# Performance work log

Measured on AMD Instinct MI355X. Metric: run time of the kernel, lower is better.

Reference implementation:

```python
import jax, jax.numpy as jnp
import numpy as np

B, T = 512, 64
STOCH, DETER, HIDDEN = 30, 200, 200
A, EMBED = 12, 1024
MIN_STD = 0.1
UPDATE_BIAS = -1.0


def _linear_init(key, fan_in, fan_out):
    w_key, b_key = jax.random.split(key)
    lim = 1.0 / np.sqrt(fan_in)
    W = jax.random.uniform(w_key, (fan_in, fan_out), minval=-lim, maxval=lim, dtype=jnp.float32)
    b = jax.random.uniform(b_key, (fan_out,), minval=-lim, maxval=lim, dtype=jnp.float32)
    return W, b


def setup_inputs() -> dict:
    key = jax.random.key(0)
    ks = jax.random.split(key, 12)
    embed = jax.random.normal(ks[0], (B, T, EMBED), dtype=jnp.float32)
    action = jax.random.normal(ks[1], (B, T, A), dtype=jnp.float32)
    noise_prior = jax.random.normal(ks[2], (B, T, STOCH), dtype=jnp.float32)
    noise_post = jax.random.normal(ks[3], (B, T, STOCH), dtype=jnp.float32)
    inp_W, inp_b = _linear_init(ks[4], STOCH + A, HIDDEN)          # _inp_layers
    gru_W, gru_b = _linear_init(ks[5], HIDDEN + DETER, 3 * DETER)  # GRUCell._layer
    img_out_W, img_out_b = _linear_init(ks[6], DETER, HIDDEN)      # _img_out_layers
    ims_W, ims_b = _linear_init(ks[7], HIDDEN, 2 * STOCH)          # _ims_stat_layer
    obs_out_W, obs_out_b = _linear_init(ks[8], DETER + EMBED, HIDDEN)  # _obs_out_layers
    obs_W, obs_b = _linear_init(ks[9], HIDDEN, 2 * STOCH)          # _obs_stat_layer
    return dict(embed=embed, action=action, noise_prior=noise_prior, noise_post=noise_post,
                inp_W=inp_W, inp_b=inp_b, gru_W=gru_W, gru_b=gru_b,
                img_out_W=img_out_W, img_out_b=img_out_b, ims_W=ims_W, ims_b=ims_b,
                obs_out_W=obs_out_W, obs_out_b=obs_out_b, obs_W=obs_W, obs_b=obs_b)


def _observe(embed, action, noise_prior, noise_post,
             inp_W, inp_b, gru_W, gru_b, img_out_W, img_out_b,
             ims_W, ims_b, obs_out_W, obs_out_b, obs_W, obs_b):
    # time-major for scan: [T, B, ...]
    emb_t = jnp.swapaxes(embed, 0, 1)
    act_t = jnp.swapaxes(action, 0, 1)
    npr_t = jnp.swapaxes(noise_prior, 0, 1)
    npo_t = jnp.swapaxes(noise_post, 0, 1)

    def step(carry, xs):
        stoch, deter = carry                    # posterior stoch [B,STOCH], deter [B,DETER]
        a, e, nz_pr, nz_po = xs
        # img_step: input MLP
        x = jax.nn.elu(jnp.concatenate([stoch, a], -1) @ inp_W + inp_b)
        # GRUCell (norm=False)
        parts = jnp.concatenate([x, deter], -1) @ gru_W + gru_b   # [B, 3*DETER]
        reset, cand, update = jnp.split(parts, 3, -1)
        reset = jax.nn.sigmoid(reset)
        cand = jnp.tanh(reset * cand)
        update = jax.nn.sigmoid(update + UPDATE_BIAS)
        deter_new = update * cand + (1.0 - update) * deter
        # prior stats
        h = jax.nn.elu(deter_new @ img_out_W + img_out_b)
        mean_pr, std_pr = jnp.split(h @ ims_W + ims_b, 2, -1)
        std_pr = jax.nn.softplus(std_pr) + MIN_STD
        stoch_pr = mean_pr + std_pr * nz_pr
        # posterior (temp_post=True): cat(deter, embed)
        ho = jax.nn.elu(jnp.concatenate([deter_new, e], -1) @ obs_out_W + obs_out_b)
        mean_po, std_po = jnp.split(ho @ obs_W + obs_b, 2, -1)
        std_po = jax.nn.softplus(std_po) + MIN_STD
        stoch_po = mean_po + std_po * nz_po
        out = (stoch_po, mean_po, std_po, stoch_pr, mean_pr, std_pr, deter_new)
        return (stoch_po, deter_new), out

    init = (jnp.zeros((B, STOCH), jnp.float32), jnp.zeros((B, DETER), jnp.float32))
    _, outs = jax.lax.scan(step, init, (act_t, emb_t, npr_t, npo_t))
    # back to batch-major and pack into a single array [B, T, 6*STOCH + DETER]
    outs = [jnp.swapaxes(o, 0, 1) for o in outs]
    return jnp.concatenate(outs, -1)


def reference(embed, action, noise_prior, noise_post,
              inp_W, inp_b, gru_W, gru_b, img_out_W, img_out_b,
              ims_W, ims_b, obs_out_W, obs_out_b, obs_W, obs_b):
    return _observe(embed, action, noise_prior, noise_post,
                    inp_W, inp_b, gru_W, gru_b, img_out_W, img_out_b,
                    ims_W, ims_b, obs_out_W, obs_out_b, obs_W, obs_b)
```

## Files before the change

### kernel.cpp

```cpp
#include <hip/hip_runtime.h>

typedef _Float16 h2   __attribute__((ext_vector_type(2)));
typedef _Float16 h4   __attribute__((ext_vector_type(4)));
typedef _Float16 half8 __attribute__((ext_vector_type(8)));
typedef float f32x4   __attribute__((ext_vector_type(4)));

#define MFMA16(a,b,c) __builtin_amdgcn_mfma_f32_16x16x32_f16((a),(b),(c),0,0,0)
#define ATOMIC_ST(p,v) __hip_atomic_store((p),(v),__ATOMIC_RELAXED,__HIP_MEMORY_SCOPE_AGENT)
#define ATOMIC_LD(p)   __hip_atomic_load((p),__ATOMIC_RELAXED,__HIP_MEMORY_SCOPE_AGENT)
#define BAR_LDS() do { asm volatile("s_waitcnt lgkmcnt(0)" ::: "memory"); \
                       __builtin_amdgcn_s_barrier();                      \
                       asm volatile("" ::: "memory"); } while (0)


#define EP_HALVES ((size_t)32768*208)

__global__ void prep_frags(const float* __restrict__ inpW, const float* __restrict__ gruW,
                           const float* __restrict__ imgW, const float* __restrict__ obsoutW,
                           const float* __restrict__ imsW, const float* __restrict__ obsW,
                           _Float16* __restrict__ frags) {
    int gb = blockIdx.x, lane = threadIdx.x;
    const float* src; int KS, K, N, ld, roff = 0, local;
    if (gb < 26)       { src = inpW;    KS = 2;  K = 42;   N = 200; ld = 200; local = gb; }
    else if (gb < 520) { src = gruW;    KS = 13; K = 400;  N = 600; ld = 600; local = gb - 26; }
    else if (gb < 611) { src = imgW;    KS = 7;  K = 200;  N = 200; ld = 200; local = gb - 520; }
    else if (gb < 702) { src = obsoutW; KS = 7;  K = 200;  N = 200; ld = 200; local = gb - 611; }
    else if (gb < 730) { src = imsW;    KS = 7;  K = 200;  N = 60;  ld = 60;  local = gb - 702; }
    else if (gb < 758) { src = obsW;    KS = 7;  K = 200;  N = 60;  ld = 60;  local = gb - 730; }
    else               { src = obsoutW; KS = 32; K = 1024; N = 200; ld = 200; roff = 200; local = gb - 758; }
    int nt = local / KS, ks = local % KS;
    int n  = nt * 16 + (lane & 15);
    int k0 = ks * 32 + (lane >> 4) * 8;
    half8 v;
#pragma unroll
    for (int j = 0; j < 8; ++j) {
        int k = k0 + j;
        float f = (k < K && n < N) ? src[(size_t)(k + roff) * ld + n] : 0.0f;
        v[j] = (_Float16)f;
    }
    *(half8*)(frags + (size_t)gb * 512 + lane * 8) = v;
}

__global__ __launch_bounds__(256) void ep_gemm(const float* __restrict__ embed,
                                               const _Float16* __restrict__ w2f,
                                               _Float16* __restrict__ ep) {
    __shared__ __align__(16) _Float16 aE[16 * 1048];
    int tid = threadIdx.x;
    int rb = blockIdx.x * 16;
#pragma unroll
    for (int i = 0; i < 16; ++i) {
        float4 e = *((const float4*)(embed + (size_t)(rb + i) * 1024) + tid);
        h4 hv; hv[0] = (_Float16)e.x; hv[1] = (_Float16)e.y; hv[2] = (_Float16)e.z; hv[3] = (_Float16)e.w;
        *(h4*)(aE + i * 1048 + tid * 4) = hv;
    }
    __syncthreads();
    int w = tid >> 6, lane = tid & 63, m = lane & 15, q = lane >> 4;
    f32x4 acc[4] = {};
    int nts[4]; int ntc = 0;
    for (int nt = w; nt < 13; nt += 4) nts[ntc++] = nt;
    half8 bb[2][4];
#pragma unroll
    for (int j = 0; j < 4; ++j) if (j < ntc)
        bb[0][j] = *(const half8*)(w2f + ((size_t)(nts[j] * 32) * 64 + lane) * 8);
#pragma unroll
    for (int ks = 0; ks < 32; ++ks) {
        int cur = ks & 1, nxt = cur ^ 1;
        if (ks < 31) {
#pragma unroll
            for (int j = 0; j < 4; ++j) if (j < ntc)
                bb[nxt][j] = *(const half8*)(w2f + ((size_t)(nts[j] * 32 + ks + 1) * 64 + lane) * 8);
        }
        half8 a = *(const half8*)(aE + m * 1048 + ks * 32 + q * 8);
#pragma unroll
        for (int j = 0; j < 4; ++j) if (j < ntc)
            acc[j] = MFMA16(a, bb[cur][j], acc[j]);
    }
    for (int j = 0; j < ntc; ++j) {
        int col = nts[j] * 16 + m;
#pragma unroll
        for (int i = 0; i < 4; ++i)
            ep[(size_t)(rb + q * 4 + i) * 208 + col] = (_Float16)acc[j][i];
    }
}

__device__ __forceinline__ float sigm_(float x) { return 1.0f / (1.0f + __expf(-x)); }
__device__ __forceinline__ float tanh_(float x) { float e = __expf(2.0f * x); return 1.0f - 2.0f / (e + 1.0f); }
__device__ __forceinline__ float elu_(float x)  { return x > 0.0f ? x : __expf(x) - 1.0f; }
__device__ __forceinline__ float sp_(float x)   { return fmaxf(x, 0.0f) + log1pf(__expf(-fabsf(x))); }
__device__ __forceinline__ unsigned packh2(float a, float b) {
    h2 p; p[0] = (_Float16)a; p[1] = (_Float16)b;
    return __builtin_bit_cast(unsigned, p);
}

__global__ __launch_bounds__(512) __attribute__((amdgpu_waves_per_eu(2, 2))) void rssm_scan(
    const float* __restrict__ action, const float* __restrict__ npr, const float* __restrict__ npo,
    const float* __restrict__ inp_b, const float* __restrict__ gru_b,
    const float* __restrict__ img_b, const float* __restrict__ obsout_b,
    const float* __restrict__ ims_b, const float* __restrict__ obs_b,
    const _Float16* __restrict__ frags, const _Float16* __restrict__ ep,
    unsigned* __restrict__ qdet, unsigned* __restrict__ stochb,
    unsigned* __restrict__ flags, float* __restrict__ out) {

    __shared__ __align__(16) unsigned actI[16 * 36];
    __shared__ __align__(16) unsigned actG[16 * 212];
    __shared__ __align__(16) unsigned actX[16 * 116];
    __shared__ __align__(16) _Float16 parts[16 * 208];
    __shared__ float statspre[16 * 65];
    __shared__ float bias[1320];

    const _Float16* Finp  = frags;
    const _Float16* Fgru  = frags + (size_t)26  * 512;
    const _Float16* Fimg  = frags + (size_t)520 * 512;
    const _Float16* Fobsd = frags + (size_t)611 * 512;
    const _Float16* Fims  = frags + (size_t)702 * 512;
    const _Float16* Fobs  = frags + (size_t)730 * 512;

    const int tid = threadIdx.x, w = tid >> 6, lane = tid & 63, m = lane & 15, q = lane >> 4;
    const int g = blockIdx.x & 31, wg = blockIdx.x >> 5;
    const int rb = g * 16;
    const bool post = (wg >= 2);
    const bool statside = (wg == 0) || (wg == 2);
    const int colA = w * 16 + m;
    const int colB = (8 + w) * 16 + m;
    unsigned* gf = flags + g * 512;

    for (int i = tid; i < 1320; i += 512) {
        float v;
        if (i < 200) v = inp_b[i];
        else if (i < 800)  v = gru_b[i - 200];
        else if (i < 1000) v = img_b[i - 800];
        else if (i < 1200) v = obsout_b[i - 1000];
        else if (i < 1260) v = ims_b[i - 1200];
        else               v = obs_b[i - 1260];
        bias[i] = v;
    }
    for (int i = tid; i < 16 * 36;  i += 512) actI[i] = 0u;
    for (int i = tid; i < 16 * 212; i += 512) actG[i] = 0u;
    for (int i = tid; i < 16 * 116; i += 512) actX[i] = 0u;

    half8 bgru0[13];
    {
        int tA = (w < 4) ? (3 * wg + w) : (12 + 3 * wg + (w - 4));
#pragma unroll
        for (int ks = 0; ks < 13; ++ks)
            bgru0[ks] = *(const half8*)(Fgru + ((size_t)(tA * 13 + ks) * 64 + lane) * 8);
    }
    half8 bgru1[13];
    if (w < 4) {
        int tB = 25 + 3 * wg + w;
#pragma unroll
        for (int ks = 0; ks < 13; ++ks)
            bgru1[ks] = *(const half8*)(Fgru + ((size_t)(tB * 13 + ks) * 64 + lane) * 8);
    }
    half8 bi0[2], bi1[2];
#pragma unroll
    for (int ks = 0; ks < 2; ++ks)
        bi0[ks] = *(const half8*)(Finp + ((size_t)(w * 2 + ks) * 64 + lane) * 8);
    if (w < 5) {
#pragma unroll
        for (int ks = 0; ks < 2; ++ks)
            bi1[ks] = *(const half8*)(Finp + ((size_t)((8 + w) * 2 + ks) * 64 + lane) * 8);
    }
    const _Float16* F3 = post ? Fobsd : Fimg;
    const _Float16* F4 = post ? Fobs : Fims;
    half8 bp3a[7];
    if (statside) {
#pragma unroll
        for (int ks = 0; ks < 7; ++ks)
            bp3a[ks] = *(const half8*)(F3 + ((size_t)(w * 7 + ks) * 64 + lane) * 8);
    }
    half8 bp4[7];
    if (statside && w >= 4) {
#pragma unroll
        for (int ks = 0; ks < 7; ++ks)
            bp4[ks] = *(const half8*)(F4 + ((size_t)((w - 4) * 7 + ks) * 64 + lane) * 8);
    }
    __syncthreads();

    for (int t = 0; t < 64; ++t) {
        h2 epA[4], epB[4];
        if (post && !(m & 1)) {
#pragma unroll
            for (int i = 0; i < 4; ++i)
                epA[i] = *(const h2*)(ep + ((size_t)(rb + q * 4 + i) * 64 + t) * 208 + colA);
            if (w < 5 && colB < 200) {
#pragma unroll
                for (int i = 0; i < 4; ++i)
                    epB[i] = *(const h2*)(ep + ((size_t)(rb + q * 4 + i) * 64 + t) * 208 + colB);
            }
        }

        if (t > 0 && wg != 2) {
            if (tid == 0) {
                unsigned* f = gf + (t - 1) * 8 + 4;
                int it = 0;
                while (ATOMIC_LD(f) != (unsigned)t) {
                    __builtin_amdgcn_s_sleep(1);
                    if (++it > (1 << 20)) break;
                }
            }
            BAR_LDS();
            __atomic_signal_fence(__ATOMIC_ACQUIRE);
            if (tid < 240) {
                int r = tid / 15, cp = tid % 15;
                actI[r * 36 + cp] =
                    ATOMIC_LD(stochb + (size_t)((((t - 1) & 1) * 32 + g)) * 256 + r * 16 + cp);
            }
        }
        if (tid < 96) {
            int r = tid / 6, cp = tid % 6;
            float2 a2 = *(const float2*)(action + ((size_t)(rb + r) * 64 + t) * 12 + 2 * cp);
            actI[r * 36 + 15 + cp] = packh2(a2.x, a2.y);
        }
        float2 nz = make_float2(0.0f, 0.0f);
        if (statside && tid < 240) {
            int r = tid / 15, cp = tid % 15;
            const float* ns = post ? npo : npr;
            nz = *(const float2*)(ns + ((size_t)(rb + r) * 64 + t) * 30 + 2 * cp);
        }
        BAR_LDS();

        {
            f32x4 acc = {}, acc2 = {};
#pragma unroll
            for (int ks = 0; ks < 2; ++ks) {
                half8 a = *(const half8*)(actI + m * 36 + ks * 16 + q * 4);
                acc = MFMA16(a, bi0[ks], acc);
                if (w < 5) acc2 = MFMA16(a, bi1[ks], acc2);
            }
            f32x4 accN;
#pragma unroll
            for (int i = 0; i < 4; ++i) accN[i] = __shfl_xor(acc[i], 1);
            if (!(m & 1)) {
                int col = w * 16 + m;
#pragma unroll
                for (int i = 0; i < 4; ++i)
                    actG[(q * 4 + i) * 212 + (col >> 1)] =
                        packh2(elu_(acc[i] + bias[col]), elu_(accN[i] + bias[col + 1]));
            }
            if (w < 5) {
                f32x4 acc2N;
#pragma unroll
                for (int i = 0; i < 4; ++i) acc2N[i] = __shfl_xor(acc2[i], 1);
                if (!(m & 1)) {
                    int col = (8 + w) * 16 + m;
                    if (col < 200) {
#pragma unroll
                        for (int i = 0; i < 4; ++i)
                            actG[(q * 4 + i) * 212 + (col >> 1)] =
                                packh2(elu_(acc2[i] + bias[col]), elu_(acc2N[i] + bias[col + 1]));
                    }
                }
            }
        }
        BAR_LDS();

        {
            f32x4 a0 = {}, a1 = {};
#pragma unroll
            for (int ks = 0; ks < 13; ++ks) {
                half8 a = *(const half8*)(actG + m * 212 + ks * 16 + q * 4);
                a0 = MFMA16(a, bgru0[ks], a0);
                if (w < 4) a1 = MFMA16(a, bgru1[ks], a1);
            }
#pragma unroll
            for (int i = 0; i < 4; ++i)
                parts[(q * 4 + i) * 208 + w * 16 + m] = (_Float16)a0[i];
            if (w < 4) {
#pragma unroll
                for (int i = 0; i < 4; ++i)
                    parts[(q * 4 + i) * 208 + (8 + w) * 16 + m] = (_Float16)a1[i];
            }
        }
        half8 pf3[7];
        if (statside && w < 5) {
#pragma unroll
            for (int ks = 0; ks < 7; ++ks)
                pf3[ks] = *(const half8*)(F3 + ((size_t)((8 + w) * 7 + ks) * 64 + lane) * 8);
        }
        BAR_LDS();

        unsigned* qd = qdet + (size_t)((t & 1) * 32 + g) * 1600;
        float gdn0 = 0.0f, gdn1 = 0.0f; int gr = 0, gn0 = 0;
        if (tid < 400) {
            int r = tid / 25, p = tid % 25;
            int n0 = 50 * wg + 2 * p;
            float pg[3][2];
#pragma unroll
            for (int j = 0; j < 3; ++j) {
                int cg = n0 + 200 * j;
                int bj = (j == 0) ? 3 * wg : (j == 1) ? 12 + 3 * wg : 25 + 3 * wg;
                int lt = 4 * j + (cg >> 4) - bj;
                h2 v = *(const h2*)(parts + r * 208 + lt * 16 + (cg & 15));
                pg[j][0] = (float)v[0] + bias[200 + cg];
                pg[j][1] = (float)v[1] + bias[200 + cg + 1];
            }
            h2 dold = *(const h2*)&actG[r * 212 + 100 + (n0 >> 1)];
            float dn[2];
#pragma unroll
            for (int e = 0; e < 2; ++e) {
                float reset = sigm_(pg[0][e]);
                float cand  = tanh_(reset * pg[1][e]);
                float upd   = sigm_(pg[2][e] - 1.0f);
                dn[e] = upd * cand + (1.0f - upd) * (float)dold[e];
            }
            unsigned pk = packh2(dn[0], dn[1]);
            actG[r * 212 + 100 + (n0 >> 1)] = pk;
            ATOMIC_ST(qd + r * 100 + (n0 >> 1), pk);
            gdn0 = dn[0]; gdn1 = dn[1]; gr = r; gn0 = n0;
        }
        __syncthreads();

        __atomic_signal_fence(__ATOMIC_RELEASE);
        if (tid == 0) ATOMIC_ST(gf + t * 8 + wg, (unsigned)(t + 1));
        if (tid < 400)
            *(float2*)(out + ((size_t)(rb + gr) * 64 + t) * 380 + 180 + gn0) = make_float2(gdn0, gdn1);
        if (tid < 3) {
            unsigned* f = gf + t * 8 + ((wg + 1 + tid) & 3);
            int it = 0;
            while (ATOMIC_LD(f) != (unsigned)(t + 1)) {
                __builtin_amdgcn_s_sleep(1);
                if (++it > (1 << 20)) break;
            }
        }
        BAR_LDS();
        __atomic_signal_fence(__ATOMIC_ACQUIRE);
        for (int i = tid; i < 1200; i += 512) {
            int r = i / 75, idx = i % 75;
            int pp = (25 * (wg + 1) + idx) % 100;
            actG[r * 212 + 100 + pp] = ATOMIC_LD(qd + r * 100 + pp);
        }
        BAR_LDS();

        if (statside) {
            f32x4 acc = {}, acc2 = {};
#pragma unroll
            for (int ks = 0; ks < 7; ++ks) {
                half8 a = *(const half8*)(actG + m * 212 + 100 + ks * 16 + q * 4);
                acc = MFMA16(a, bp3a[ks], acc);
                if (w < 5) acc2 = MFMA16(a, pf3[ks], acc2);
            }
            f32x4 accN;
#pragma unroll
            for (int i = 0; i < 4; ++i) accN[i] = __shfl_xor(acc[i], 1);
            if (!(m & 1)) {
                int bb0 = post ? 1000 : 800;
#pragma unroll
                for (int i = 0; i < 4; ++i) {
                    float e0 = post ? (float)epA[i][0] : 0.0f;
                    float e1 = post ? (float)epA[i][1] : 0.0f;
                    actX[(q * 4 + i) * 116 + (colA >> 1)] =
                        packh2(elu_(acc[i] + bias[bb0 + colA] + e0),
                               elu_(accN[i] + bias[bb0 + colA + 1] + e1));
                }
            }
            if (w < 5) {
                f32x4 acc2N;
#pragma unroll
                for (int i = 0; i < 4; ++i) acc2N[i] = __shfl_xor(acc2[i], 1);
                if (!(m & 1) && colB < 200) {
                    int bb0 = post ? 1000 : 800;
#pragma unroll
                    for (int i = 0; i < 4; ++i) {
                        float e0 = post ? (float)epB[i][0] : 0.0f;
                        float e1 = post ? (float)epB[i][1] : 0.0f;
                        actX[(q * 4 + i) * 116 + (colB >> 1)] =
                            packh2(elu_(acc2[i] + bias[bb0 + colB] + e0),
                                   elu_(acc2N[i] + bias[bb0 + colB + 1] + e1));
                    }
                }
            }
        }
        BAR_LDS();

        if (statside && w >= 4) {
            f32x4 acc = {};
#pragma unroll
            for (int ks = 0; ks < 7; ++ks) {
                half8 a = *(const half8*)(actX + m * 116 + ks * 16 + q * 4);
                acc = MFMA16(a, bp4[ks], acc);
            }
#pragma unroll
            for (int i = 0; i < 4; ++i)
                statspre[(q * 4 + i) * 65 + (w - 4) * 16 + m] = acc[i];
        }
        BAR_LDS();

        float o0v = 0.f, o1v = 0.f, o2v = 0.f, o3v = 0.f, o4v = 0.f, o5v = 0.f;
        int pr = 0, pcp = 0; bool doout = false;
        if (statside && tid < 240) {
            int r = tid / 15, cp = tid % 15;
            int bb0 = post ? 1260 : 1200;
            float m0 = statspre[r * 65 + 2 * cp]     + bias[bb0 + 2 * cp];
            float m1 = statspre[r * 65 + 2 * cp + 1] + bias[bb0 + 2 * cp + 1];
            float s0 = sp_(statspre[r * 65 + 30 + 2 * cp]     + bias[bb0 + 30 + 2 * cp]) + 0.1f;
            float s1 = sp_(statspre[r * 65 + 30 + 2 * cp + 1] + bias[bb0 + 30 + 2 * cp + 1]) + 0.1f;
            float st0 = m0 + s0 * nz.x, st1 = m1 + s1 * nz.y;
            if (post) {
                unsigned pk = packh2(st0, st1);
                actI[r * 36 + cp] = pk;
                ATOMIC_ST(stochb + (size_t)((t & 1) * 32 + g) * 256 + r * 16 + cp, pk);
            }
            o0v = st0; o1v = st1; o2v = m0; o3v = m1; o4v = s0; o5v = s1;
            pr = r; pcp = cp; doout = true;
        }
        __syncthreads();
        if (wg == 2 && t < 63) {
            __atomic_signal_fence(__ATOMIC_RELEASE);
            if (tid == 0) ATOMIC_ST(gf + t * 8 + 4, (unsigned)(t + 1));
        }
        if (doout) {
            size_t ob = ((size_t)(rb + pr) * 64 + t) * 380;
            int o0 = post ? 0 : 90;
            *(float2*)(out + ob + o0 + 2 * pcp)      = make_float2(o0v, o1v);
            *(float2*)(out + ob + o0 + 30 + 2 * pcp) = make_float2(o2v, o3v);
            *(float2*)(out + ob + o0 + 60 + 2 * pcp) = make_float2(o4v, o5v);
        }
    }
}

extern "C" void kernel_launch(void* const* d_in, const int* in_sizes, int n_in,
                              void* d_out, int out_size, void* d_ws, size_t ws_size,
                              hipStream_t stream) {
    const float* embed   = (const float*)d_in[0];
    const float* action  = (const float*)d_in[1];
    const float* npr     = (const float*)d_in[2];
    const float* npo     = (const float*)d_in[3];
    const float* inpW    = (const float*)d_in[4];
    const float* inpb    = (const float*)d_in[5];
    const float* gruW    = (const float*)d_in[6];
    const float* grub    = (const float*)d_in[7];
    const float* imgW    = (const float*)d_in[8];
    const float* imgb    = (const float*)d_in[9];
    const float* imsW    = (const float*)d_in[10];
    const float* imsb    = (const float*)d_in[11];
    const float* obsoutW = (const float*)d_in[12];
    const float* obsoutb = (const float*)d_in[13];
    const float* obsW    = (const float*)d_in[14];
    const float* obsb    = (const float*)d_in[15];

    char* ws = (char*)d_ws;
    _Float16* ep     = (_Float16*)ws;
    _Float16* frags  = (_Float16*)(ws + EP_HALVES * 2);
    char* p          = ws + EP_HALVES * 2 + (size_t)1174 * 1024;
    unsigned* qdetb  = (unsigned*)p;
    p += (size_t)2 * 32 * 1600 * 4;
    unsigned* stochb = (unsigned*)p;
    p += (size_t)2 * 32 * 256 * 4;
    unsigned* flags  = (unsigned*)p;

    prep_frags<<<1174, 64, 0, stream>>>(inpW, gruW, imgW, obsoutW, imsW, obsW, frags);
    ep_gemm<<<2048, 256, 0, stream>>>(embed, frags + (size_t)758 * 512, ep);
    rssm_scan<<<128, 512, 0, stream>>>(action, npr, npo, inpb, grub, imgb, obsoutb,
                                       imsb, obsb, frags, ep, qdetb, stochb, flags,
                                       (float*)d_out);
}
```

Before: 948.8 us.

## Move prior branch to dedicated workgroups and compute posterior redundantly in all GRU groups

Workgroups grow from 128 to 160. The four GRU workgroups per batch group now each compute the posterior stoch path themselves, so the stochb exchange and its wait go away from the critical recurrence. A fifth workgroup per group computes the prior (img_out and ims) off the critical path, reading deter from qdet and signalling a flag so the buffer can be reused. The ep buffer stride also shrinks from 208 to 200 halves. The trade-off is redundant posterior math in every GRU workgroup and an extra polling dependency on the prior workgroup for double-buffer safety.

```diff
diff --git a/kernel.cpp b/kernel.cpp
--- a/kernel.cpp
+++ b/kernel.cpp
@@ -13,7 +13,7 @@
                        asm volatile("" ::: "memory"); } while (0)
 
 
-#define EP_HALVES ((size_t)32768*208)
+#define EP_HALVES ((size_t)32768*200)
 
 __global__ void prep_frags(const float* __restrict__ inpW, const float* __restrict__ gruW,
                            const float* __restrict__ imgW, const float* __restrict__ obsoutW,
@@ -77,9 +77,11 @@
     }
     for (int j = 0; j < ntc; ++j) {
         int col = nts[j] * 16 + m;
-#pragma unroll
-        for (int i = 0; i < 4; ++i)
-            ep[(size_t)(rb + q * 4 + i) * 208 + col] = (_Float16)acc[j][i];
+        if (col < 200) {
+#pragma unroll
+            for (int i = 0; i < 4; ++i)
+                ep[(size_t)(rb + q * 4 + i) * 200 + col] = (_Float16)acc[j][i];
+        }
     }
 }
 
@@ -98,8 +100,8 @@
     const float* __restrict__ img_b, const float* __restrict__ obsout_b,
     const float* __restrict__ ims_b, const float* __restrict__ obs_b,
     const _Float16* __restrict__ frags, const _Float16* __restrict__ ep,
-    unsigned* __restrict__ qdet, unsigned* __restrict__ stochb,
-    unsigned* __restrict__ flags, float* __restrict__ out) {
+    unsigned* __restrict__ qdet, unsigned* __restrict__ flags,
+    float* __restrict__ out) {
 
     __shared__ __align__(16) unsigned actI[16 * 36];
     __shared__ __align__(16) unsigned actG[16 * 212];
@@ -118,8 +120,6 @@
     const int tid = threadIdx.x, w = tid >> 6, lane = tid & 63, m = lane & 15, q = lane >> 4;
     const int g = blockIdx.x & 31, wg = blockIdx.x >> 5;
     const int rb = g * 16;
-    const bool post = (wg >= 2);
-    const bool statside = (wg == 0) || (wg == 2);
     const int colA = w * 16 + m;
     const int colB = (8 + w) * 16 + m;
     unsigned* gf = flags + g * 512;
@@ -138,283 +138,356 @@
     for (int i = tid; i < 16 * 212; i += 512) actG[i] = 0u;
     for (int i = tid; i < 16 * 116; i += 512) actX[i] = 0u;
 
-    half8 bgru0[13];
-    {
-        int tA = (w < 4) ? (3 * wg + w) : (12 + 3 * wg + (w - 4));
-#pragma unroll
-        for (int ks = 0; ks < 13; ++ks)
-            bgru0[ks] = *(const half8*)(Fgru + ((size_t)(tA * 13 + ks) * 64 + lane) * 8);
-    }
-    half8 bgru1[13];
-    if (w < 4) {
-        int tB = 25 + 3 * wg + w;
-#pragma unroll
-        for (int ks = 0; ks < 13; ++ks)
-            bgru1[ks] = *(const half8*)(Fgru + ((size_t)(tB * 13 + ks) * 64 + lane) * 8);
-    }
-    half8 bi0[2], bi1[2];
-#pragma unroll
-    for (int ks = 0; ks < 2; ++ks)
-        bi0[ks] = *(const half8*)(Finp + ((size_t)(w * 2 + ks) * 64 + lane) * 8);
-    if (w < 5) {
+    if (wg < 4) {
+        half8 bgru0[13];
+        {
+            int tA = (w < 4) ? (3 * wg + w) : (12 + 3 * wg + (w - 4));
+#pragma unroll
+            for (int ks = 0; ks < 13; ++ks)
+                bgru0[ks] = *(const half8*)(Fgru + ((size_t)(tA * 13 + ks) * 64 + lane) * 8);
+        }
+        half8 bgru1[13];
+        if (w < 4) {
+            int tB = 25 + 3 * wg + w;
+#pragma unroll
+            for (int ks = 0; ks < 13; ++ks)
+                bgru1[ks] = *(const half8*)(Fgru + ((size_t)(tB * 13 + ks) * 64 + lane) * 8);
+        }
+        half8 bi0[2], bi1[2];
 #pragma unroll
         for (int ks = 0; ks < 2; ++ks)
-            bi1[ks] = *(const half8*)(Finp + ((size_t)((8 + w) * 2 + ks) * 64 + lane) * 8);
-    }
-    const _Float16* F3 = post ? Fobsd : Fimg;
-    const _Float16* F4 = post ? Fobs : Fims;
-    half8 bp3a[7];
-    if (statside) {
+            bi0[ks] = *(const half8*)(Finp + ((size_t)(w * 2 + ks) * 64 + lane) * 8);
+        if (w < 5) {
+#pragma unroll
+            for (int ks = 0; ks < 2; ++ks)
+                bi1[ks] = *(const half8*)(Finp + ((size_t)((8 + w) * 2 + ks) * 64 + lane) * 8);
+        }
+        half8 bp3a[7];
 #pragma unroll
         for (int ks = 0; ks < 7; ++ks)
-            bp3a[ks] = *(const half8*)(F3 + ((size_t)(w * 7 + ks) * 64 + lane) * 8);
-    }
-    half8 bp4[7];
-    if (statside && w >= 4) {
-#pragma unroll
-        for (int ks = 0; ks < 7; ++ks)
-            bp4[ks] = *(const half8*)(F4 + ((size_t)((w - 4) * 7 + ks) * 64 + lane) * 8);
-    }
-    __syncthreads();
-
-    for (int t = 0; t < 64; ++t) {
-        h2 epA[4], epB[4];
-        if (post && !(m & 1)) {
-#pragma unroll
-            for (int i = 0; i < 4; ++i)
-                epA[i] = *(const h2*)(ep + ((size_t)(rb + q * 4 + i) * 64 + t) * 208 + colA);
-            if (w < 5 && colB < 200) {
+            bp3a[ks] = *(const half8*)(Fobsd + ((size_t)(w * 7 + ks) * 64 + lane) * 8);
+        half8 bp4[7];
+        if (w >= 4) {
+#pragma unroll
+            for (int ks = 0; ks < 7; ++ks)
+                bp4[ks] = *(const half8*)(Fobs + ((size_t)((w - 4) * 7 + ks) * 64 + lane) * 8);
+        }
+        __syncthreads();
+
+        unsigned wg4pf = 0u;
+        for (int t = 0; t < 64; ++t) {
+            h2 epA[4], epB[4];
+            if (!(m & 1)) {
 #pragma unroll
                 for (int i = 0; i < 4; ++i)
-                    epB[i] = *(const h2*)(ep + ((size_t)(rb + q * 4 + i) * 64 + t) * 208 + colB);
-            }
-        }
-
-        if (t > 0 && wg != 2) {
-            if (tid == 0) {
-                unsigned* f = gf + (t - 1) * 8 + 4;
+                    epA[i] = *(const h2*)(ep + ((size_t)(rb + q * 4 + i) * 64 + t) * 200 + colA);
+                if (w < 5 && colB < 200) {
+#pragma unroll
+                    for (int i = 0; i < 4; ++i)
+                        epB[i] = *(const h2*)(ep + ((size_t)(rb + q * 4 + i) * 64 + t) * 200 + colB);
+                }
+            }
+            float2 a2 = make_float2(0.0f, 0.0f);
+            if (tid < 96) {
+                int r = tid / 6, cp = tid % 6;
+                a2 = *(const float2*)(action + ((size_t)(rb + r) * 64 + t) * 12 + 2 * cp);
+            }
+            float2 nz = make_float2(0.0f, 0.0f);
+            if (tid < 240) {
+                int r = tid / 15, cp = tid % 15;
+                nz = *(const float2*)(npo + ((size_t)(rb + r) * 64 + t) * 30 + 2 * cp);
+            }
+            if (t >= 2 && tid == 3 && wg4pf < (unsigned)(t - 1)) {
                 int it = 0;
-                while (ATOMIC_LD(f) != (unsigned)t) {
+                unsigned v = ATOMIC_LD(gf + 508);
+                while (v < (unsigned)(t - 1)) {
+                    __builtin_amdgcn_s_sleep(1);
+                    v = ATOMIC_LD(gf + 508);
+                    if (++it > (1 << 20)) break;
+                }
+                wg4pf = v;
+            }
+            if (tid < 96) {
+                int r = tid / 6, cp = tid % 6;
+                actI[r * 36 + 15 + cp] = packh2(a2.x, a2.y);
+            }
+            BAR_LDS();
+
+            {
+                f32x4 acc = {}, acc2 = {};
+#pragma unroll
+                for (int ks = 0; ks < 2; ++ks) {
+                    half8 a = *(const half8*)(actI + m * 36 + ks * 16 + q * 4);
+                    acc = MFMA16(a, bi0[ks], acc);
+                    if (w < 5) acc2 = MFMA16(a, bi1[ks], acc2);
+                }
+                f32x4 accN;
+#pragma unroll
+                for (int i = 0; i < 4; ++i) accN[i] = __shfl_xor(acc[i], 1);
+                if (!(m & 1)) {
+                    int col = w * 16 + m;
+#pragma unroll
+                    for (int i = 0; i < 4; ++i)
+                        actG[(q * 4 + i) * 212 + (col >> 1)] =
+                            packh2(elu_(acc[i] + bias[col]), elu_(accN[i] + bias[col + 1]));
+                }
+                if (w < 5) {
+                    f32x4 acc2N;
+#pragma unroll
+                    for (int i = 0; i < 4; ++i) acc2N[i] = __shfl_xor(acc2[i], 1);
+                    if (!(m & 1)) {
+                        int col = (8 + w) * 16 + m;
+                        if (col < 200) {
+#pragma unroll
+                            for (int i = 0; i < 4; ++i)
+                                actG[(q * 4 + i) * 212 + (col >> 1)] =
+                                    packh2(elu_(acc2[i] + bias[col]), elu_(acc2N[i] + bias[col + 1]));
+                        }
+                    }
+                }
+            }
+            BAR_LDS();
+
+            {
+                f32x4 a0 = {}, a1 = {};
+#pragma unroll
+                for (int ks = 0; ks < 13; ++ks) {
+                    half8 a = *(const half8*)(actG + m * 212 + ks * 16 + q * 4);
+                    a0 = MFMA16(a, bgru0[ks], a0);
+                    if (w < 4) a1 = MFMA16(a, bgru1[ks], a1);
+                }
+#pragma unroll
+                for (int i = 0; i < 4; ++i)
+                    parts[(q * 4 + i) * 208 + w * 16 + m] = (_Float16)a0[i];
+                if (w < 4) {
+#pragma unroll
+                    for (int i = 0; i < 4; ++i)
+                        parts[(q * 4 + i) * 208 + (8 + w) * 16 + m] = (_Float16)a1[i];
+                }
+            }
+            half8 pf3[7];
+            if (w < 5) {
+#pragma unroll
+                for (int ks = 0; ks < 7; ++ks)
+                    pf3[ks] = *(const half8*)(Fobsd + ((size_t)((8 + w) * 7 + ks) * 64 + lane) * 8);
+            }
+            BAR_LDS();
+
+            unsigned* qd = qdet + (size_t)((t & 1) * 32 + g) * 1600;
+            float gdn0 = 0.0f, gdn1 = 0.0f; int gr = 0, gn0 = 0;
+            if (tid < 400) {
+                int r = tid / 25, p = tid % 25;
+                int n0 = 50 * wg + 2 * p;
+                float pg[3][2];
+#pragma unroll
+                for (int j = 0; j < 3; ++j) {
+                    int cg = n0 + 200 * j;
+                    int bj = (j == 0) ? 3 * wg : (j == 1) ? 12 + 3 * wg : 25 + 3 * wg;
+                    int lt = 4 * j + (cg >> 4) - bj;
+                    h2 v = *(const h2*)(parts + r * 208 + lt * 16 + (cg & 15));
+                    pg[j][0] = (float)v[0] + bias[200 + cg];
+                    pg[j][1] = (float)v[1] + bias[200 + cg + 1];
+                }
+                h2 dold = *(const h2*)&actG[r * 212 + 100 + (n0 >> 1)];
+                float dn[2];
+#pragma unroll
+                for (int e = 0; e < 2; ++e) {
+                    float reset = sigm_(pg[0][e]);
+                    float cand  = tanh_(reset * pg[1][e]);
+                    float upd   = sigm_(pg[2][e] - 1.0f);
+                    dn[e] = upd * cand + (1.0f - upd) * (float)dold[e];
+                }
+                unsigned pk = packh2(dn[0], dn[1]);
+                actG[r * 212 + 100 + (n0 >> 1)] = pk;
+                ATOMIC_ST(qd + r * 100 + (n0 >> 1), pk);
+                gdn0 = dn[0]; gdn1 = dn[1]; gr = r; gn0 = n0;
+            }
+            __syncthreads();
+
+            __atomic_signal_fence(__ATOMIC_RELEASE);
+            if (tid == 0) ATOMIC_ST(gf + t * 8 + wg, (unsigned)(t + 1));
+            if (tid < 400)
+                *(float2*)(out + ((size_t)(rb + gr) * 64 + t) * 380 + 180 + gn0) = make_float2(gdn0, gdn1);
+            if (tid < 3) {
+                unsigned* f = gf + t * 8 + ((wg + 1 + tid) & 3);
+                int it = 0;
+                while (ATOMIC_LD(f) != (unsigned)(t + 1)) {
                     __builtin_amdgcn_s_sleep(1);
                     if (++it > (1 << 20)) break;
                 }
             }
             BAR_LDS();
             __atomic_signal_fence(__ATOMIC_ACQUIRE);
+            for (int i = tid; i < 1200; i += 512) {
+                int r = i / 75, idx = i % 75;
+                int pp = (25 * (wg + 1) + idx) % 100;
+                actG[r * 212 + 100 + pp] = ATOMIC_LD(qd + r * 100 + pp);
+            }
+            if (tid == 3) wg4pf = ATOMIC_LD(gf + 508);
+            BAR_LDS();
+
+            {
+                f32x4 acc = {}, acc2 = {};
+#pragma unroll
+                for (int ks = 0; ks < 7; ++ks) {
+                    half8 a = *(const half8*)(actG + m * 212 + 100 + ks * 16 + q * 4);
+                    acc = MFMA16(a, bp3a[ks], acc);
+                    if (w < 5) acc2 = MFMA16(a, pf3[ks], acc2);
+                }
+                f32x4 accN;
+#pragma unroll
+                for (int i = 0; i < 4; ++i) accN[i] = __shfl_xor(acc[i], 1);
+                if (!(m & 1)) {
+#pragma unroll
+                    for (int i = 0; i < 4; ++i)
+                        actX[(q * 4 + i) * 116 + (colA >> 1)] =
+                            packh2(elu_(acc[i] + bias[1000 + colA] + (float)epA[i][0]),
+                                   elu_(accN[i] + bias[1000 + colA + 1] + (float)epA[i][1]));
+                }
+                if (w < 5) {
+                    f32x4 acc2N;
+#pragma unroll
+                    for (int i = 0; i < 4; ++i) acc2N[i] = __shfl_xor(acc2[i], 1);
+                    if (!(m & 1) && colB < 200) {
+#pragma unroll
+                        for (int i = 0; i < 4; ++i)
+                            actX[(q * 4 + i) * 116 + (colB >> 1)] =
+                                packh2(elu_(acc2[i] + bias[1000 + colB] + (float)epB[i][0]),
+                                       elu_(acc2N[i] + bias[1000 + colB + 1] + (float)epB[i][1]));
+                    }
+                }
+            }
+            BAR_LDS();
+
+            if (w >= 4) {
+                f32x4 acc = {};
+#pragma unroll
+                for (int ks = 0; ks < 7; ++ks) {
+                    half8 a = *(const half8*)(actX + m * 116 + ks * 16 + q * 4);
+                    acc = MFMA16(a, bp4[ks], acc);
+                }
+#pragma unroll
+                for (int i = 0; i < 4; ++i)
+                    statspre[(q * 4 + i) * 65 + (w - 4) * 16 + m] = acc[i];
+            }
+            BAR_LDS();
+
             if (tid < 240) {
                 int r = tid / 15, cp = tid % 15;
-                actI[r * 36 + cp] =
-                    ATOMIC_LD(stochb + (size_t)((((t - 1) & 1) * 32 + g)) * 256 + r * 16 + cp);
-            }
-        }
-        if (tid < 96) {
-            int r = tid / 6, cp = tid % 6;
-            float2 a2 = *(const float2*)(action + ((size_t)(rb + r) * 64 + t) * 12 + 2 * cp);
-            actI[r * 36 + 15 + cp] = packh2(a2.x, a2.y);
-        }
-        float2 nz = make_float2(0.0f, 0.0f);
-        if (statside && tid < 240) {
-            int r = tid / 15, cp = tid % 15;
-            const float* ns = post ? npo : npr;
-            nz = *(const float2*)(ns + ((size_t)(rb + r) * 64 + t) * 30 + 2 * cp);
-        }
-        BAR_LDS();
-
-        {
-            f32x4 acc = {}, acc2 = {};
-#pragma unroll
-            for (int ks = 0; ks < 2; ++ks) {
-                half8 a = *(const half8*)(actI + m * 36 + ks * 16 + q * 4);
-                acc = MFMA16(a, bi0[ks], acc);
-                if (w < 5) acc2 = MFMA16(a, bi1[ks], acc2);
-            }
-            f32x4 accN;
-#pragma unroll
-            for (int i = 0; i < 4; ++i) accN[i] = __shfl_xor(acc[i], 1);
-            if (!(m & 1)) {
-                int col = w * 16 + m;
+                float m0 = statspre[r * 65 + 2 * cp]     + bias[1260 + 2 * cp];
+                float m1 = statspre[r * 65 + 2 * cp + 1] + bias[1260 + 2 * cp + 1];
+                float s0 = sp_(statspre[r * 65 + 30 + 2 * cp]     + bias[1260 + 30 + 2 * cp]) + 0.1f;
+                float s1 = sp_(statspre[r * 65 + 30 + 2 * cp + 1] + bias[1260 + 30 + 2 * cp + 1]) + 0.1f;
+                float st0 = m0 + s0 * nz.x, st1 = m1 + s1 * nz.y;
+                actI[r * 36 + cp] = packh2(st0, st1);
+                if (wg == 2) {
+                    size_t ob = ((size_t)(rb + r) * 64 + t) * 380;
+                    *(float2*)(out + ob + 2 * cp)      = make_float2(st0, st1);
+                    *(float2*)(out + ob + 30 + 2 * cp) = make_float2(m0, m1);
+                    *(float2*)(out + ob + 60 + 2 * cp) = make_float2(s0, s1);
+                }
+            }
+        }
+    } else {
+        half8 bp3a[7];
+#pragma unroll
+        for (int ks = 0; ks < 7; ++ks)
+            bp3a[ks] = *(const half8*)(Fimg + ((size_t)(w * 7 + ks) * 64 + lane) * 8);
+        half8 bp3b[7];
+        if (w < 5) {
+#pragma unroll
+            for (int ks = 0; ks < 7; ++ks)
+                bp3b[ks] = *(const half8*)(Fimg + ((size_t)((8 + w) * 7 + ks) * 64 + lane) * 8);
+        }
+        half8 bp4[7];
+        if (w >= 4) {
+#pragma unroll
+            for (int ks = 0; ks < 7; ++ks)
+                bp4[ks] = *(const half8*)(Fims + ((size_t)((w - 4) * 7 + ks) * 64 + lane) * 8);
+        }
+        __syncthreads();
+
+        for (int t = 0; t < 64; ++t) {
+            float2 nz = make_float2(0.0f, 0.0f);
+            if (tid < 240) {
+                int r = tid / 15, cp = tid % 15;
+                nz = *(const float2*)(npr + ((size_t)(rb + r) * 64 + t) * 30 + 2 * cp);
+            }
+            if (tid < 4) {
+                unsigned* f = gf + t * 8 + tid;
+                int it = 0;
+                while (ATOMIC_LD(f) != (unsigned)(t + 1)) {
+                    __builtin_amdgcn_s_sleep(1);
+                    if (++it > (1 << 20)) break;
+                }
+            }
+            BAR_LDS();
+            __atomic_signal_fence(__ATOMIC_ACQUIRE);
+            const unsigned* qd = qdet + (size_t)((t & 1) * 32 + g) * 1600;
+            for (int i = tid; i < 1600; i += 512)
+                actG[(i / 100) * 212 + 100 + (i % 100)] = ATOMIC_LD(qd + i);
+            BAR_LDS();
+            __atomic_signal_fence(__ATOMIC_RELEASE);
+            if (tid == 0) ATOMIC_ST(gf + 508, (unsigned)(t + 1));
+
+            {
+                f32x4 acc = {}, acc2 = {};
+#pragma unroll
+                for (int ks = 0; ks < 7; ++ks) {
+                    half8 a = *(const half8*)(actG + m * 212 + 100 + ks * 16 + q * 4);
+                    acc = MFMA16(a, bp3a[ks], acc);
+                    if (w < 5) acc2 = MFMA16(a, bp3b[ks], acc2);
+                }
+                f32x4 accN;
+#pragma unroll
+                for (int i = 0; i < 4; ++i) accN[i] = __shfl_xor(acc[i], 1);
+                if (!(m & 1)) {
+#pragma unroll
+                    for (int i = 0; i < 4; ++i)
+                        actX[(q * 4 + i) * 116 + (colA >> 1)] =
+                            packh2(elu_(acc[i] + bias[800 + colA]),
+                                   elu_(accN[i] + bias[800 + colA + 1]));
+                }
+                if (w < 5) {
+                    f32x4 acc2N;
+#pragma unroll
+                    for (int i = 0; i < 4; ++i) acc2N[i] = __shfl_xor(acc2[i], 1);
+                    if (!(m & 1) && colB < 200) {
+#pragma unroll
+                        for (int i = 0; i < 4; ++i)
+                            actX[(q * 4 + i) * 116 + (colB >> 1)] =
+                                packh2(elu_(acc2[i] + bias[800 + colB]),
+                                       elu_(acc2N[i] + bias[800 + colB + 1]));
+                    }
+                }
+            }
+            BAR_LDS();
+
+            if (w >= 4) {
+                f32x4 acc = {};
+#pragma unroll
+                for (int ks = 0; ks < 7; ++ks) {
+                    half8 a = *(const half8*)(actX + m * 116 + ks * 16 + q * 4);
+                    acc = MFMA16(a, bp4[ks], acc);
+                }
 #pragma unroll
                 for (int i = 0; i < 4; ++i)
-                    actG[(q * 4 + i) * 212 + (col >> 1)] =
-                        packh2(elu_(acc[i] + bias[col]), elu_(accN[i] + bias[col + 1]));
-            }
-            if (w < 5) {
-                f32x4 acc2N;
-#pragma unroll
-                for (int i = 0; i < 4; ++i) acc2N[i] = __shfl_xor(acc2[i], 1);
-                if (!(m & 1)) {
-                    int col = (8 + w) * 16 + m;
-                    if (col < 200) {
-#pragma unroll
-                        for (int i = 0; i < 4; ++i)
-                            actG[(q * 4 + i) * 212 + (col >> 1)] =
-                                packh2(elu_(acc2[i] + bias[col]), elu_(acc2N[i] + bias[col + 1]));
-                    }
-                }
-            }
-        }
-        BAR_LDS();
-
-        {
-            f32x4 a0 = {}, a1 = {};
-#pragma unroll
-            for (int ks = 0; ks < 13; ++ks) {
-                half8 a = *(const half8*)(actG + m * 212 + ks * 16 + q * 4);
-                a0 = MFMA16(a, bgru0[ks], a0);
-                if (w < 4) a1 = MFMA16(a, bgru1[ks], a1);
-            }
-#pragma unroll
-            for (int i = 0; i < 4; ++i)
-                parts[(q * 4 + i) * 208 + w * 16 + m] = (_Float16)a0[i];
-            if (w < 4) {
-#pragma unroll
-                for (int i = 0; i < 4; ++i)
-                    parts[(q * 4 + i) * 208 + (8 + w) * 16 + m] = (_Float16)a1[i];
-            }
-        }
-        half8 pf3[7];
-        if (statside && w < 5) {
-#pragma unroll
-            for (int ks = 0; ks < 7; ++ks)
-                pf3[ks] = *(const half8*)(F3 + ((size_t)((8 + w) * 7 + ks) * 64 + lane) * 8);
-        }
-        BAR_LDS();
-
-        unsigned* qd = qdet + (size_t)((t & 1) * 32 + g) * 1600;
-        float gdn0 = 0.0f, gdn1 = 0.0f; int gr = 0, gn0 = 0;
-        if (tid < 400) {
-            int r = tid / 25, p = tid % 25;
-            int n0 = 50 * wg + 2 * p;
-            float pg[3][2];
-#pragma unroll
-            for (int j = 0; j < 3; ++j) {
-                int cg = n0 + 200 * j;
-                int bj = (j == 0) ? 3 * wg : (j == 1) ? 12 + 3 * wg : 25 + 3 * wg;
-                int lt = 4 * j + (cg >> 4) - bj;
-                h2 v = *(const h2*)(parts + r * 208 + lt * 16 + (cg & 15));
-                pg[j][0] = (float)v[0] + bias[200 + cg];
-                pg[j][1] = (float)v[1] + bias[200 + cg + 1];
-            }
-            h2 dold = *(const h2*)&actG[r * 212 + 100 + (n0 >> 1)];
-            float dn[2];
-#pragma unroll
-            for (int e = 0; e < 2; ++e) {
-                float reset = sigm_(pg[0][e]);
-                float cand  = tanh_(reset * pg[1][e]);
-                float upd   = sigm_(pg[2][e] - 1.0f);
-                dn[e] = upd * cand + (1.0f - upd) * (float)dold[e];
-            }
-            unsigned pk = packh2(dn[0], dn[1]);
-            actG[r * 212 + 100 + (n0 >> 1)] = pk;
-            ATOMIC_ST(qd + r * 100 + (n0 >> 1), pk);
-            gdn0 = dn[0]; gdn1 = dn[1]; gr = r; gn0 = n0;
-        }
-        __syncthreads();
-
-        __atomic_signal_fence(__ATOMIC_RELEASE);
-        if (tid == 0) ATOMIC_ST(gf + t * 8 + wg, (unsigned)(t + 1));
-        if (tid < 400)
-            *(float2*)(out + ((size_t)(rb + gr) * 64 + t) * 380 + 180 + gn0) = make_float2(gdn0, gdn1);
-        if (tid < 3) {
-            unsigned* f = gf + t * 8 + ((wg + 1 + tid) & 3);
-            int it = 0;
-            while (ATOMIC_LD(f) != (unsigned)(t + 1)) {
-                __builtin_amdgcn_s_sleep(1);
-                if (++it > (1 << 20)) break;
-            }
-        }
-        BAR_LDS();
-        __atomic_signal_fence(__ATOMIC_ACQUIRE);
-        for (int i = tid; i < 1200; i += 512) {
-            int r = i / 75, idx = i % 75;
-            int pp = (25 * (wg + 1) + idx) % 100;
-            actG[r * 212 + 100 + pp] = ATOMIC_LD(qd + r * 100 + pp);
-        }
-        BAR_LDS();
-
-        if (statside) {
-            f32x4 acc = {}, acc2 = {};
-#pragma unroll
-            for (int ks = 0; ks < 7; ++ks) {
-                half8 a = *(const half8*)(actG + m * 212 + 100 + ks * 16 + q * 4);
-                acc = MFMA16(a, bp3a[ks], acc);
-                if (w < 5) acc2 = MFMA16(a, pf3[ks], acc2);
-            }
-            f32x4 accN;
-#pragma unroll
-            for (int i = 0; i < 4; ++i) accN[i] = __shfl_xor(acc[i], 1);
-            if (!(m & 1)) {
-                int bb0 = post ? 1000 : 800;
-#pragma unroll
-                for (int i = 0; i < 4; ++i) {
-                    float e0 = post ? (float)epA[i][0] : 0.0f;
-                    float e1 = post ? (float)epA[i][1] : 0.0f;
-                    actX[(q * 4 + i) * 116 + (colA >> 1)] =
-                        packh2(elu_(acc[i] + bias[bb0 + colA] + e0),
-                               elu_(accN[i] + bias[bb0 + colA + 1] + e1));
-                }
-            }
-            if (w < 5) {
-                f32x4 acc2N;
-#pragma unroll
-                for (int i = 0; i < 4; ++i) acc2N[i] = __shfl_xor(acc2[i], 1);
-                if (!(m & 1) && colB < 200) {
-                    int bb0 = post ? 1000 : 800;
-#pragma unroll
-                    for (int i = 0; i < 4; ++i) {
-                        float e0 = post ? (float)epB[i][0] : 0.0f;
-                        float e1 = post ? (float)epB[i][1] : 0.0f;
-                        actX[(q * 4 + i) * 116 + (colB >> 1)] =
-                            packh2(elu_(acc2[i] + bias[bb0 + colB] + e0),
-                                   elu_(acc2N[i] + bias[bb0 + colB + 1] + e1));
-                    }
-                }
-            }
-        }
-        BAR_LDS();
-
-        if (statside && w >= 4) {
-            f32x4 acc = {};
-#pragma unroll
-            for (int ks = 0; ks < 7; ++ks) {
-                half8 a = *(const half8*)(actX + m * 116 + ks * 16 + q * 4);
-                acc = MFMA16(a, bp4[ks], acc);
-            }
-#pragma unroll
-            for (int i = 0; i < 4; ++i)
-                statspre[(q * 4 + i) * 65 + (w - 4) * 16 + m] = acc[i];
-        }
-        BAR_LDS();
-
-        float o0v = 0.f, o1v = 0.f, o2v = 0.f, o3v = 0.f, o4v = 0.f, o5v = 0.f;
-        int pr = 0, pcp = 0; bool doout = false;
-        if (statside && tid < 240) {
-            int r = tid / 15, cp = tid % 15;
-            int bb0 = post ? 1260 : 1200;
-            float m0 = statspre[r * 65 + 2 * cp]     + bias[bb0 + 2 * cp];
-            float m1 = statspre[r * 65 + 2 * cp + 1] + bias[bb0 + 2 * cp + 1];
-            float s0 = sp_(statspre[r * 65 + 30 + 2 * cp]     + bias[bb0 + 30 + 2 * cp]) + 0.1f;
-            float s1 = sp_(statspre[r * 65 + 30 + 2 * cp + 1] + bias[bb0 + 30 + 2 * cp + 1]) + 0.1f;
-            float st0 = m0 + s0 * nz.x, st1 = m1 + s1 * nz.y;
-            if (post) {
-                unsigned pk = packh2(st0, st1);
-                actI[r * 36 + cp] = pk;
-                ATOMIC_ST(stochb + (size_t)((t & 1) * 32 + g) * 256 + r * 16 + cp, pk);
-            }
-            o0v = st0; o1v = st1; o2v = m0; o3v = m1; o4v = s0; o5v = s1;
-            pr = r; pcp = cp; doout = true;
-        }
-        __syncthreads();
-        if (wg == 2 && t < 63) {
-            __atomic_signal_fence(__ATOMIC_RELEASE);
-            if (tid == 0) ATOMIC_ST(gf + t * 8 + 4, (unsigned)(t + 1));
-        }
-        if (doout) {
-            size_t ob = ((size_t)(rb + pr) * 64 + t) * 380;
-            int o0 = post ? 0 : 90;
-            *(float2*)(out + ob + o0 + 2 * pcp)      = make_float2(o0v, o1v);
-            *(float2*)(out + ob + o0 + 30 + 2 * pcp) = make_float2(o2v, o3v);
-            *(float2*)(out + ob + o0 + 60 + 2 * pcp) = make_float2(o4v, o5v);
+                    statspre[(q * 4 + i) * 65 + (w - 4) * 16 + m] = acc[i];
+            }
+            BAR_LDS();
+
+            if (tid < 240) {
+                int r = tid / 15, cp = tid % 15;
+                float m0 = statspre[r * 65 + 2 * cp]     + bias[1200 + 2 * cp];
+                float m1 = statspre[r * 65 + 2 * cp + 1] + bias[1200 + 2 * cp + 1];
+                float s0 = sp_(statspre[r * 65 + 30 + 2 * cp]     + bias[1200 + 30 + 2 * cp]) + 0.1f;
+                float s1 = sp_(statspre[r * 65 + 30 + 2 * cp + 1] + bias[1200 + 30 + 2 * cp + 1]) + 0.1f;
+                float st0 = m0 + s0 * nz.x, st1 = m1 + s1 * nz.y;
+                size_t ob = ((size_t)(rb + r) * 64 + t) * 380;
+                *(float2*)(out + ob + 90 + 2 * cp)  = make_float2(st0, st1);
+                *(float2*)(out + ob + 120 + 2 * cp) = make_float2(m0, m1);
+                *(float2*)(out + ob + 150 + 2 * cp) = make_float2(s0, s1);
+            }
         }
     }
 }
@@ -445,13 +518,11 @@
     char* p          = ws + EP_HALVES * 2 + (size_t)1174 * 1024;
     unsigned* qdetb  = (unsigned*)p;
     p += (size_t)2 * 32 * 1600 * 4;
-    unsigned* stochb = (unsigned*)p;
-    p += (size_t)2 * 32 * 256 * 4;
-    unsigned* flags  = (unsigned*)p;
+    unsigned* flagsb = (unsigned*)p;
 
     prep_frags<<<1174, 64, 0, stream>>>(inpW, gruW, imgW, obsoutW, imsW, obsW, frags);
     ep_gemm<<<2048, 256, 0, stream>>>(embed, frags + (size_t)758 * 512, ep);
-    rssm_scan<<<128, 512, 0, stream>>>(action, npr, npo, inpb, grub, imgb, obsoutb,
-                                       imsb, obsb, frags, ep, qdetb, stochb, flags,
+    rssm_scan<<<160, 512, 0, stream>>>(action, npr, npo, inpb, grub, imgb, obsoutb,
+                                       imsb, obsb, frags, ep, qdetb, flagsb,
                                        (float*)d_out);
 }
```

Measured after the change: 844.3 us. 1.12x faster.
